# Kernel optimization log

Hardware: AMD Instinct MI355X
Metric: run time of the kernel (lower is better)

Reference implementation:

```python
import jax, jax.numpy as jnp
import numpy as np

B, P, K, F, H = 128, 200, 60, 4, 64   # events, points/event, knn k, feat dim, hidden
N = B * P


def setup_inputs() -> dict:
    key = jax.random.key(0)
    k0, k1, k2, k3 = jax.random.split(key, 4)
    x = jax.random.normal(k0, (N, F), jnp.float32)
    pos = jax.random.normal(k1, (N, 3), jnp.float32)
    batch = jnp.arange(N, dtype=jnp.int32) // P  # sorted event ids, equal-size events
    W1 = jax.random.normal(k2, (F + 3, H), jnp.float32) / np.sqrt(F + 3)
    b1 = jnp.zeros((H,), jnp.float32)
    W2 = jax.random.normal(k3, (H, H), jnp.float32) / np.sqrt(H)
    b2 = jnp.zeros((H,), jnp.float32)
    return {"x": x, "pos": pos, "batch": batch, "W1": W1, "b1": b1, "W2": W2, "b2": b2}


def _knn_edges(pos):
    """knn_graph(pos, K, batch, loop=False, flow='source_to_target').
    Equal-size events -> batched [B,P,P] pairwise distances, no cross-event edges."""
    p = pos.reshape(B, P, 3)
    d2 = jnp.sum((p[:, :, None, :] - p[:, None, :, :]) ** 2, axis=-1)  # [B,P,P]
    d2 = d2 + jnp.eye(P, dtype=d2.dtype) * 1e10                        # exclude self (loop=False)
    _, nbr = jax.lax.top_k(-d2, K)                                     # [B,P,K] local neighbor ids
    src = (nbr + (jnp.arange(B, dtype=nbr.dtype) * P)[:, None, None]).reshape(-1)  # sources j
    dst = jnp.repeat(jnp.arange(N, dtype=src.dtype), K)                             # targets i
    return jnp.stack([src, dst])  # [2, N*K]


def _local_nn(m, W1, b1, W2, b2):
    h = jax.nn.relu(m @ W1 + b1)
    return jax.nn.relu(h @ W2 + b2)


def reference(x, pos, batch, W1, b1, W2, b2):
    edge_index = _knn_edges(pos)
    src, dst = edge_index[0], edge_index[1]
    # PointConv message: net(concat[x_j, pos_j - pos_i]) on each edge
    rel = pos[src] - pos[dst]                             # [E,3]
    m = jnp.concatenate([x[src], rel], axis=-1)           # [E,F+3]
    h = _local_nn(m, W1, b1, W2, b2)                      # [E,H]
    out = h.reshape(N, K, H).max(axis=1)                  # max-aggregate per target node
    # PyG PointConv adds self-loops by default: message with rel = 0
    m_self = jnp.concatenate([x, jnp.zeros((N, 3), x.dtype)], axis=-1)
    h_self = _local_nn(m_self, W1, b1, W2, b2)            # [N,H]
    out = jnp.maximum(out, h_self)
    return (out, pos, batch, edge_index)
```

## Files before the change

### kernel.cpp

```cpp
#include <hip/hip_runtime.h>
#include <hip/hip_bf16.h>

typedef unsigned short ushort_t;
typedef unsigned int u32;
typedef unsigned long long u64;
typedef __attribute__((ext_vector_type(8))) short bf16x8;
typedef __attribute__((ext_vector_type(4))) float f32x4;
typedef __attribute__((ext_vector_type(4))) u32 u32x4;

#define NB 128
#define PP 200
#define KK 60
#define NN (NB*PP)
#define HH 64

#define OUT_OFF   0
#define POS_OFF   (NN*HH)
#define BATCH_OFF (POS_OFF + NN*3)
#define ESRC_OFF  (BATCH_OFF + NN)
#define EDST_OFF  (ESRC_OFF + NN*KK)

static __device__ __forceinline__ ushort_t f2bf(float f) {
    __hip_bfloat16 h = __float2bfloat16(f);
    ushort_t u; __builtin_memcpy(&u, &h, 2); return u;
}
static __device__ __forceinline__ u32 packtr(float a, float b) {
    return __builtin_amdgcn_perm(__float_as_uint(b), __float_as_uint(a), 0x07060302u);
}
static __device__ __forceinline__ u32 prefix_lt(u64 b) {
    return __builtin_amdgcn_mbcnt_hi((u32)(b >> 32),
                                     __builtin_amdgcn_mbcnt_lo((u32)b, 0));
}

__global__ __launch_bounds__(256) void fused_kernel(const float* __restrict__ x,
                                                    const float* __restrict__ pos,
                                                    const float* __restrict__ W1,
                                                    const float* __restrict__ b1p,
                                                    const float* __restrict__ W2,
                                                    const float* __restrict__ b2p,
                                                    float* __restrict__ out) {
    __shared__ alignas(16) float xs[PP * 4];
    __shared__ alignas(16) float psl[PP * 3];
    __shared__ alignas(16) u32 jslot[4 * 128];
    __shared__ alignas(16) u32 msg[4 * 256];
    __shared__ alignas(16) u32 af[4 * 512];

    int tid = threadIdx.x, blk = blockIdx.x;
    int e = blk / 25;
    int pl0b = (blk % 25) * 8;
    int i0b  = e * PP + pl0b;

    if (tid < 200) ((f32x4*)xs)[tid]  = ((const f32x4*)x)[e * PP + tid];
    if (tid < 150) ((f32x4*)psl)[tid] = ((const f32x4*)pos)[e * 150 + tid];
    __syncthreads();

    if (tid < 24) out[POS_OFF + i0b * 3 + tid] = psl[pl0b * 3 + tid];
    if (tid < 8)  out[BATCH_OFF + i0b + tid] = (float)e;

    int lane = tid & 63, wv = tid >> 6;
    int lo16 = lane & 15, hi16 = lane >> 4;
    int plA = pl0b + wv * 2, plB = plA + 1;
    int iA = e * PP + plA,   iB = iA + 1;

    float axA = psl[plA*3], ayA = psl[plA*3+1], azA = psl[plA*3+2];
    float axB = psl[plB*3], ayB = psl[plB*3+1], azB = psl[plB*3+2];

    u32 keyA[4], keyB[4];
    #pragma unroll
    for (int q = 0; q < 4; ++q) {
        int j = lane + q * 64;
        int jc = (j < PP) ? j : 0;
        float px = psl[jc*3], py = psl[jc*3+1], pz = psl[jc*3+2];
        float dxA = px-axA, dyA = py-ayA, dzA = pz-azA;
        float dxB = px-axB, dyB = py-ayB, dzB = pz-azB;
        float d2A = dxA*dxA + dyA*dyA + dzA*dzA;
        float d2B = dxB*dxB + dyB*dyB + dzB*dzB;
        keyA[q] = (j < PP && j != plA)
                ? ((__float_as_uint(d2A) & 0xFFFFFF00u) | (u32)j) : 0xFFFFFFFFu;
        keyB[q] = (j < PP && j != plB)
                ? ((__float_as_uint(d2B) & 0xFFFFFF00u) | (u32)j) : 0xFFFFFFFFu;
    }

    u32 loA = 0u, hiA = 0xFFFFFFFFu, loB = 0u, hiB = 0xFFFFFFFFu;
    for (int it = 0; it < 32; ++it) {
        u32 mA = loA + ((hiA - loA) >> 1);
        u32 mB = loB + ((hiB - loB) >> 1);
        int cA = __builtin_popcountll(__ballot(keyA[0] < mA))
               + __builtin_popcountll(__ballot(keyA[1] < mA))
               + __builtin_popcountll(__ballot(keyA[2] < mA))
               + __builtin_popcountll(__ballot(keyA[3] < mA));
        int cB = __builtin_popcountll(__ballot(keyB[0] < mB))
               + __builtin_popcountll(__ballot(keyB[1] < mB))
               + __builtin_popcountll(__ballot(keyB[2] < mB))
               + __builtin_popcountll(__ballot(keyB[3] < mB));
        if (cA >= KK) hiA = mA; else loA = mA;
        if (cB >= KK) hiB = mB; else loB = mB;
    }

    const int jsb = wv * 128;
    if (lane >= KK) {
        jslot[jsb + lane]      = (u32)plA;
        jslot[jsb + 64 + lane] = (u32)plB;
    }
    #pragma unroll
    for (int t = 0; t < 2; ++t) {
        const u32* key = t ? keyB : keyA;
        u32 hh = t ? hiB : hiA;
        int i  = t ? iB : iA;
        u64 m0 = __ballot(key[0] < hh);
        u64 m1 = __ballot(key[1] < hh);
        u64 m2 = __ballot(key[2] < hh);
        u64 m3 = __ballot(key[3] < hh);
        u32 s1 = (u32)__builtin_popcountll(m0);
        u32 s2 = s1 + (u32)__builtin_popcountll(m1);
        u32 s3 = s2 + (u32)__builtin_popcountll(m2);
        u32 sl[4] = { prefix_lt(m0), s1 + prefix_lt(m1),
                      s2 + prefix_lt(m2), s3 + prefix_lt(m3) };
        #pragma unroll
        for (int q = 0; q < 4; ++q) {
            if (key[q] < hh) {
                u32 j = key[q] & 0xFFu;
                out[ESRC_OFF + i * KK + (int)sl[q]] = (float)(e * PP + (int)j);
                jslot[jsb + t * 64 + (int)sl[q]] = j;
            }
        }
        if (lane < KK) out[EDST_OFF + i * KK + lane] = (float)i;
    }

    bf16x8 w1f[4];
    #pragma unroll
    for (int th = 0; th < 4; ++th) {
        bf16x8 v = (bf16x8)0;
        if (hi16 == 0) {
            #pragma unroll
            for (int j = 0; j < 8; ++j) {
                float w = (j < 7) ? W1[j * 64 + th * 16 + lo16] : b1p[th * 16 + lo16];
                v[j] = (short)f2bf(w);
            }
        }
        w1f[th] = v;
    }
    bf16x8 bfr[4][2];
    #pragma unroll
    for (int t = 0; t < 4; ++t)
        #pragma unroll
        for (int s = 0; s < 2; ++s)
            #pragma unroll
            for (int j = 0; j < 8; ++j)
                bfr[t][s][j] = (short)f2bf(W2[(s*32 + hi16*8 + j) * 64 + t*16 + lo16]);
    float b2v[4];
    #pragma unroll
    for (int t = 0; t < 4; ++t) b2v[t] = b2p[t * 16 + lo16];

    const int msb = wv * 256;
    const int afb = wv * 512;
    for (int tl = 0; tl < 2; ++tl) {
        int i = iA + tl;
        int pl = plA + tl;
        int jloc = (int)jslot[jsb + tl * 64 + lane];
        f32x4 xv = ((const f32x4*)xs)[jloc];
        float rx = psl[jloc*3]   - psl[pl*3];
        float ry = psl[jloc*3+1] - psl[pl*3+1];
        float rz = psl[jloc*3+2] - psl[pl*3+2];
        u32x4 mrow;
        mrow[0] = packtr(xv[0], xv[1]);
        mrow[1] = packtr(xv[2], xv[3]);
        mrow[2] = packtr(rx, ry);
        mrow[3] = packtr(rz, 1.0f);
        *(u32x4*)&msg[msb + lane * 4] = mrow;

        float runmax[4] = {0.f, 0.f, 0.f, 0.f};
        #pragma unroll
        for (int rt = 0; rt < 4; ++rt) {
            union { u32 w[4]; bf16x8 v; } mu;
            *(u32x4*)mu.w = *(const u32x4*)&msg[msb + (rt * 16 + lo16) * 4];
            bf16x8 mf = (hi16 == 0) ? mu.v : (bf16x8)0;

            f32x4 c1[4];
            #pragma unroll
            for (int th = 0; th < 4; ++th)
                c1[th] = __builtin_amdgcn_mfma_f32_16x16x32_bf16(w1f[th], mf,
                                                                 (f32x4)0.f, 0, 0, 0);
            #pragma unroll
            for (int th = 0; th < 4; ++th) {
                u32 pk0 = packtr(fmaxf(c1[th][0], 0.f), fmaxf(c1[th][1], 0.f));
                u32 pk1 = packtr(fmaxf(c1[th][2], 0.f), fmaxf(c1[th][3], 0.f));
                int s = th >> 1;
                int dlane = lo16 + (((th & 1) * 2 + (hi16 >> 1)) << 4);
                int dbase = (hi16 & 1) * 2;
                af[afb + s * 256 + (dbase + 0) * 64 + dlane] = pk0;
                af[afb + s * 256 + (dbase + 1) * 64 + dlane] = pk1;
            }
            f32x4 acc[4];
            #pragma unroll
            for (int t = 0; t < 4; ++t) acc[t] = (f32x4)0.f;
            #pragma unroll
            for (int s = 0; s < 2; ++s) {
                union { u32 w[4]; bf16x8 v; } u;
                #pragma unroll
                for (int d = 0; d < 4; ++d)
                    u.w[d] = af[afb + s * 256 + d * 64 + lane];
                #pragma unroll
                for (int t = 0; t < 4; ++t)
                    acc[t] = __builtin_amdgcn_mfma_f32_16x16x32_bf16(u.v, bfr[t][s],
                                                                     acc[t], 0, 0, 0);
            }
            #pragma unroll
            for (int t = 0; t < 4; ++t) {
                #pragma unroll
                for (int reg = 0; reg < 4; ++reg)
                    runmax[t] = fmaxf(runmax[t], acc[t][reg] + b2v[t]);
            }
        }
        #pragma unroll
        for (int t = 0; t < 4; ++t) {
            runmax[t] = fmaxf(runmax[t], __shfl_xor(runmax[t], 16, 64));
            runmax[t] = fmaxf(runmax[t], __shfl_xor(runmax[t], 32, 64));
        }
        if (lane < 16) {
            #pragma unroll
            for (int t = 0; t < 4; ++t)
                out[OUT_OFF + i * 64 + t * 16 + lane] = runmax[t];
        }
    }
}

extern "C" void kernel_launch(void* const* d_in, const int* in_sizes, int n_in,
                              void* d_out, int out_size, void* d_ws, size_t ws_size,
                              hipStream_t stream) {
    const float* x     = (const float*)d_in[0];
    const float* pos   = (const float*)d_in[1];
    const float* W1    = (const float*)d_in[3];
    const float* b1    = (const float*)d_in[4];
    const float* W2    = (const float*)d_in[5];
    const float* b2    = (const float*)d_in[6];
    float* out = (float*)d_out;
    (void)d_ws; (void)ws_size; (void)in_sizes; (void)n_in; (void)out_size;

    fused_kernel<<<dim3(NN / 8), dim3(256), 0, stream>>>(x, pos, W1, b1, W2, b2, out);
}
```

Before: 114.7 us.

## Early-exit radix select, hoist bias and relu out of max, shrink LDS

The bisection search for the K-th nearest distance now starts from the +inf bit pattern and leaves the loop early once both rows find an exact count of K or the interval collapses. The b2 bias add and the final ReLU are moved out of the per-element max and applied once at the end, since max(a+b)=max(a)+b and relu is monotone. Weight conversion to bf16 now uses a pair-packing perm instead of per-element conversion. The hidden-activation staging buffer is halved by reusing one slice per s-step, and masking of the message fragment now loads from a zero row instead of using a select. These are mostly small savings in ALU work and LDS, with some risk from the data-dependent, divergent loop exit and from LDS reuse ordering within a wave.

Result: faster. 109.4 us (-4.7%).

```diff
diff --git a/kernel.cpp b/kernel.cpp
--- a/kernel.cpp
+++ b/kernel.cpp
@@ -20,10 +20,6 @@
 #define ESRC_OFF  (BATCH_OFF + NN)
 #define EDST_OFF  (ESRC_OFF + NN*KK)
 
-static __device__ __forceinline__ ushort_t f2bf(float f) {
-    __hip_bfloat16 h = __float2bfloat16(f);
-    ushort_t u; __builtin_memcpy(&u, &h, 2); return u;
-}
 static __device__ __forceinline__ u32 packtr(float a, float b) {
     return __builtin_amdgcn_perm(__float_as_uint(b), __float_as_uint(a), 0x07060302u);
 }
@@ -43,7 +39,8 @@
     __shared__ alignas(16) float psl[PP * 3];
     __shared__ alignas(16) u32 jslot[4 * 128];
     __shared__ alignas(16) u32 msg[4 * 256];
-    __shared__ alignas(16) u32 af[4 * 512];
+    __shared__ alignas(16) u32 af[4 * 256];
+    __shared__ alignas(16) u32 zrow[4];
 
     int tid = threadIdx.x, blk = blockIdx.x;
     int e = blk / 25;
@@ -52,6 +49,7 @@
 
     if (tid < 200) ((f32x4*)xs)[tid]  = ((const f32x4*)x)[e * PP + tid];
     if (tid < 150) ((f32x4*)psl)[tid] = ((const f32x4*)pos)[e * 150 + tid];
+    if (tid < 4)   zrow[tid] = 0u;
     __syncthreads();
 
     if (tid < 24) out[POS_OFF + i0b * 3 + tid] = psl[pl0b * 3 + tid];
@@ -81,7 +79,8 @@
                 ? ((__float_as_uint(d2B) & 0xFFFFFF00u) | (u32)j) : 0xFFFFFFFFu;
     }
 
-    u32 loA = 0u, hiA = 0xFFFFFFFFu, loB = 0u, hiB = 0xFFFFFFFFu;
+    u32 loA = 0u, hiA = 0x7F800000u, loB = 0u, hiB = 0x7F800000u;
+    int doneA = 0, doneB = 0;
     for (int it = 0; it < 32; ++it) {
         u32 mA = loA + ((hiA - loA) >> 1);
         u32 mB = loB + ((hiB - loB) >> 1);
@@ -93,8 +92,15 @@
                + __builtin_popcountll(__ballot(keyB[1] < mB))
                + __builtin_popcountll(__ballot(keyB[2] < mB))
                + __builtin_popcountll(__ballot(keyB[3] < mB));
-        if (cA >= KK) hiA = mA; else loA = mA;
-        if (cB >= KK) hiB = mB; else loB = mB;
+        if (!doneA) {
+            if (cA >= KK) hiA = mA; else loA = mA;
+            doneA = (cA == KK) | (hiA - loA <= 1u);
+        }
+        if (!doneB) {
+            if (cB >= KK) hiB = mB; else loB = mB;
+            doneB = (cB == KK) | (hiB - loB <= 1u);
+        }
+        if (doneA & doneB) break;
     }
 
     const int jsb = wv * 128;
@@ -130,33 +136,36 @@
     bf16x8 w1f[4];
     #pragma unroll
     for (int th = 0; th < 4; ++th) {
-        bf16x8 v = (bf16x8)0;
+        union { u32 w[4]; bf16x8 v; } u; u.w[0]=u.w[1]=u.w[2]=u.w[3]=0u;
         if (hi16 == 0) {
-            #pragma unroll
-            for (int j = 0; j < 8; ++j) {
-                float w = (j < 7) ? W1[j * 64 + th * 16 + lo16] : b1p[th * 16 + lo16];
-                v[j] = (short)f2bf(w);
-            }
-        }
-        w1f[th] = v;
+            int m = th * 16 + lo16;
+            u.w[0] = packtr(W1[0*64+m], W1[1*64+m]);
+            u.w[1] = packtr(W1[2*64+m], W1[3*64+m]);
+            u.w[2] = packtr(W1[4*64+m], W1[5*64+m]);
+            u.w[3] = packtr(W1[6*64+m], b1p[m]);
+        }
+        w1f[th] = u.v;
     }
     bf16x8 bfr[4][2];
     #pragma unroll
     for (int t = 0; t < 4; ++t)
         #pragma unroll
-        for (int s = 0; s < 2; ++s)
-            #pragma unroll
-            for (int j = 0; j < 8; ++j)
-                bfr[t][s][j] = (short)f2bf(W2[(s*32 + hi16*8 + j) * 64 + t*16 + lo16]);
+        for (int s = 0; s < 2; ++s) {
+            union { u32 w[4]; bf16x8 v; } u;
+            int col = t * 16 + lo16, kb = s * 32 + hi16 * 8;
+            #pragma unroll
+            for (int d = 0; d < 4; ++d)
+                u.w[d] = packtr(W2[(kb + 2*d) * 64 + col], W2[(kb + 2*d + 1) * 64 + col]);
+            bfr[t][s] = u.v;
+        }
     float b2v[4];
     #pragma unroll
     for (int t = 0; t < 4; ++t) b2v[t] = b2p[t * 16 + lo16];
 
     const int msb = wv * 256;
-    const int afb = wv * 512;
+    const int afb = wv * 256;
     for (int tl = 0; tl < 2; ++tl) {
-        int i = iA + tl;
-        int pl = plA + tl;
+        int i = iA + tl, pl = plA + tl;
         int jloc = (int)jslot[jsb + tl * 64 + lane];
         f32x4 xv = ((const f32x4*)xs)[jloc];
         float rx = psl[jloc*3]   - psl[pl*3];
@@ -169,37 +178,38 @@
         mrow[3] = packtr(rz, 1.0f);
         *(u32x4*)&msg[msb + lane * 4] = mrow;
 
-        float runmax[4] = {0.f, 0.f, 0.f, 0.f};
+        float rmax[4] = {-3.0e38f, -3.0e38f, -3.0e38f, -3.0e38f};
         #pragma unroll
         for (int rt = 0; rt < 4; ++rt) {
+            const u32* mp = (hi16 == 0) ? &msg[msb + (rt * 16 + lo16) * 4] : zrow;
             union { u32 w[4]; bf16x8 v; } mu;
-            *(u32x4*)mu.w = *(const u32x4*)&msg[msb + (rt * 16 + lo16) * 4];
-            bf16x8 mf = (hi16 == 0) ? mu.v : (bf16x8)0;
+            *(u32x4*)mu.w = *(const u32x4*)mp;
 
             f32x4 c1[4];
             #pragma unroll
             for (int th = 0; th < 4; ++th)
-                c1[th] = __builtin_amdgcn_mfma_f32_16x16x32_bf16(w1f[th], mf,
+                c1[th] = __builtin_amdgcn_mfma_f32_16x16x32_bf16(w1f[th], mu.v,
                                                                  (f32x4)0.f, 0, 0, 0);
-            #pragma unroll
-            for (int th = 0; th < 4; ++th) {
-                u32 pk0 = packtr(fmaxf(c1[th][0], 0.f), fmaxf(c1[th][1], 0.f));
-                u32 pk1 = packtr(fmaxf(c1[th][2], 0.f), fmaxf(c1[th][3], 0.f));
-                int s = th >> 1;
-                int dlane = lo16 + (((th & 1) * 2 + (hi16 >> 1)) << 4);
-                int dbase = (hi16 & 1) * 2;
-                af[afb + s * 256 + (dbase + 0) * 64 + dlane] = pk0;
-                af[afb + s * 256 + (dbase + 1) * 64 + dlane] = pk1;
-            }
             f32x4 acc[4];
             #pragma unroll
             for (int t = 0; t < 4; ++t) acc[t] = (f32x4)0.f;
+
             #pragma unroll
             for (int s = 0; s < 2; ++s) {
+                #pragma unroll
+                for (int thh = 0; thh < 2; ++thh) {
+                    int th = s * 2 + thh;
+                    u32 pk0 = packtr(fmaxf(c1[th][0], 0.f), fmaxf(c1[th][1], 0.f));
+                    u32 pk1 = packtr(fmaxf(c1[th][2], 0.f), fmaxf(c1[th][3], 0.f));
+                    int dlane = lo16 + ((thh * 2 + (hi16 >> 1)) << 4);
+                    int dbase = (hi16 & 1) * 2;
+                    af[afb + (dbase + 0) * 64 + dlane] = pk0;
+                    af[afb + (dbase + 1) * 64 + dlane] = pk1;
+                }
                 union { u32 w[4]; bf16x8 v; } u;
                 #pragma unroll
                 for (int d = 0; d < 4; ++d)
-                    u.w[d] = af[afb + s * 256 + d * 64 + lane];
+                    u.w[d] = af[afb + d * 64 + lane];
                 #pragma unroll
                 for (int t = 0; t < 4; ++t)
                     acc[t] = __builtin_amdgcn_mfma_f32_16x16x32_bf16(u.v, bfr[t][s],
@@ -207,20 +217,19 @@
             }
             #pragma unroll
             for (int t = 0; t < 4; ++t) {
-                #pragma unroll
-                for (int reg = 0; reg < 4; ++reg)
-                    runmax[t] = fmaxf(runmax[t], acc[t][reg] + b2v[t]);
+                rmax[t] = fmaxf(fmaxf(acc[t][0], acc[t][1]), rmax[t]);
+                rmax[t] = fmaxf(fmaxf(acc[t][2], acc[t][3]), rmax[t]);
             }
         }
         #pragma unroll
         for (int t = 0; t < 4; ++t) {
-            runmax[t] = fmaxf(runmax[t], __shfl_xor(runmax[t], 16, 64));
-            runmax[t] = fmaxf(runmax[t], __shfl_xor(runmax[t], 32, 64));
+            rmax[t] = fmaxf(rmax[t], __shfl_xor(rmax[t], 16, 64));
+            rmax[t] = fmaxf(rmax[t], __shfl_xor(rmax[t], 32, 64));
         }
         if (lane < 16) {
             #pragma unroll
             for (int t = 0; t < 4; ++t)
-                out[OUT_OFF + i * 64 + t * 16 + lane] = runmax[t];
+                out[OUT_OFF + i * 64 + t * 16 + lane] = fmaxf(rmax[t] + b2v[t], 0.f);
         }
     }
 }
```
